# Kernel optimization log

Hardware: AMD Instinct MI355X
Metric: run time of the kernel (lower is better)

The kernel has to match this reference:

```python
import jax, jax.numpy as jnp
import numpy as np

# ---- static config (mirrors init_kwargs) ----
CVAE = 16
VOCAB = 1 << CVAE
V_PATCH_NUMS = (1, 2, 4, 8, 16, 32)
SN = len(V_PATCH_NUMS)
NUM_LATENT_TOKENS = 1024
H = W = 32
BETA = 0.25
ENTROPY_WEIGHT = 0.1
INV_TEMP = 100.0          # temperature 0.01 as in entropy_loss default
EPS = 1e-5
W_SAMPLE_MIN = 1.0
W_BATCH_MAX = 1.0
QUANT_RESI = 0.5
N_PHI = 4                 # share_quant_resi=4 -> PhiPartiallyShared


def _phi_index():
    ticks = (np.linspace(1/3/N_PHI, 1 - 1/3/N_PHI, N_PHI) if N_PHI == 4
             else np.linspace(1/2/N_PHI, 1 - 1/2/N_PHI, N_PHI))
    return [int(np.argmin(np.abs(ticks - si / (SN - 1)))) for si in range(SN)]

PHI_IDX = _phi_index()


def _cubic(t, a=-0.75):  # torch bicubic kernel (a=-0.75)
    t = abs(t)
    if t <= 1.0:
        return (a + 2) * t**3 - (a + 3) * t**2 + 1.0
    if t < 2.0:
        return a * t**3 - 5 * a * t**2 + 8 * a * t - 4 * a
    return 0.0


def _up_matrix(n_in, n_out):
    # exact torch F.interpolate(mode='bicubic', align_corners=False) as a linear map
    M = np.zeros((n_out, n_in), np.float32)
    for i in range(n_out):
        x = (i + 0.5) * n_in / n_out - 0.5
        x0 = int(np.floor(x))
        for k in range(-1, 3):
            j = min(max(x0 + k, 0), n_in - 1)
            M[i, j] += _cubic(x - (x0 + k))
    return M

UP_MATS = {pn: jnp.asarray(_up_matrix(pn, H)) for pn in V_PATCH_NUMS if pn != H}


def area_down(x, pn):  # F.interpolate(mode='area') for divisor sizes == block mean
    B, C, Hh, Ww = x.shape
    return x.reshape(B, C, pn, Hh // pn, pn, Ww // pn).mean((3, 5))


def bicubic_up(x, pn):
    M = UP_MATS[pn]
    return jnp.einsum('hp,bcpq,wq->bchw', M, x, M)


def phi_apply(h, w, b):  # Phi: h*(1-r) + conv3x3(h)*r, r=0.5
    conv = jax.lax.conv_general_dilated(
        h, w, (1, 1), 'SAME', dimension_numbers=('NCHW', 'OIHW', 'NCHW'))
    conv = conv + b[None, :, None, None]
    return h * (1.0 - QUANT_RESI) + conv * QUANT_RESI


def lfq_forward(f_BChw, phi_w, phi_b):
    f = f_BChw.astype(jnp.float32)
    B, C, Hh, Ww = f.shape
    f_ng = jax.lax.stop_gradient(f)
    f_rest = f_ng
    f_hat = jnp.zeros_like(f)
    bitpos = jnp.arange(CVAE, dtype=jnp.int32)
    vq_loss = 0.0
    commit_loss = 0.0
    ent_loss = 0.0
    vocab_hit = jnp.zeros((SN, VOCAB), jnp.float32)
    for si, pn in enumerate(V_PATCH_NUMS):
        cv = 1.0  # scaler[si] = scale**si, scale=1
        last_direct = (si == SN - 1) and (pn == int(np.sqrt(NUM_LATENT_TOKENS)))
        rest = f_rest if last_direct else area_down(f_rest, pn)
        bits = (rest > 0)                                   # sign quantization
        # bits->index (channel-last order matches permute(0,2,3,1))
        idx = jnp.sum(bits.transpose(0, 2, 3, 1).astype(jnp.int32) << bitpos, axis=-1)  # (B,pn,pn)
        hit = jax.ops.segment_sum(jnp.ones((B * pn * pn,), jnp.float32),
                                  idx.reshape(-1), num_segments=VOCAB)
        vocab_hit = vocab_hit.at[si].add(hit)
        # index -> {-cv,+cv} codes: (B,pn,pn,C) -> (B,C,pn,pn)
        code_bits = ((idx[..., None] >> bitpos) & 1).astype(jnp.float32)
        h_small = ((code_bits * 2.0 - 1.0) * cv).transpose(0, 3, 1, 2)
        h = h_small if si == SN - 1 else bicubic_up(h_small, pn)
        h = phi_apply(h, phi_w[PHI_IDX[si]], phi_b[PHI_IDX[si]])
        # residual before this step, shape b (h w) 1 d
        x = (f - jax.lax.stop_gradient(f_hat)).transpose(0, 2, 3, 1).reshape(B, Hh * Ww, 1, C)
        f_hat = f_hat + h      # eval: mask all ones, ratio=1
        f_rest = f_rest - h
        # soft entropy loss (analytical per-sample, per-bit binary probabilities)
        p = jax.nn.sigmoid(-4.0 * x / cv * INV_TEMP)        # (B,HW,1,C)
        prob = jnp.stack([p, 1.0 - p], axis=-1)             # (B,HW,1,C,2)
        sample_ent = -(prob * jnp.log(prob + EPS)).sum(-1)  # per-bit entropy
        per_sample_entropy = sample_ent.sum(-1).mean()
        avg_prob = prob.mean((0, 1, 2))                     # (C,2)
        codebook_entropy = -(avg_prob * jnp.log(avg_prob + EPS)).sum()
        ent_loss = ent_loss + (W_SAMPLE_MIN * per_sample_entropy
                               - W_BATCH_MAX * codebook_entropy)
        vq_loss = vq_loss + jnp.mean((f_hat - f_ng) ** 2)
        commit_loss = commit_loss + BETA * jnp.mean((jax.lax.stop_gradient(f_hat) - f) ** 2)
    vq_loss = vq_loss / SN
    commit_loss = commit_loss / SN
    ent_loss = ent_loss * (ENTROPY_WEIGHT / SN)
    f_hat_out = jax.lax.stop_gradient(f_hat - f_ng) + f     # straight-through estimator
    total = vq_loss + commit_loss + ent_loss
    return f_hat_out, total, vocab_hit


def setup_inputs() -> dict:
    key = jax.random.key(0)
    k1, k2 = jax.random.split(key)
    f = jax.random.normal(k1, (256, 16, 32, 32), dtype=jnp.float32)
    phi_w = jax.random.normal(k2, (N_PHI, CVAE, CVAE, 3, 3), dtype=jnp.float32) * 0.05
    phi_b = jnp.zeros((N_PHI, CVAE), dtype=jnp.float32)
    return {"f_BChw": f, "phi_w": phi_w, "phi_b": phi_b}


def reference(f_BChw, phi_w, phi_b):
    return lfq_forward(f_BChw, phi_w, phi_b)
```

## Files before the change

### kernel.cpp

```cpp
#include <hip/hip_runtime.h>

#define VOCAB 65536
#define NELEM 4194304
#define BHW   262144

__device__ __forceinline__ double cubic_d(double t) {
  const double a = -0.75;
  t = fabs(t);
  if (t <= 1.0) return ((a + 2.0) * t - (a + 3.0)) * t * t + 1.0;
  if (t < 2.0)  return a * (((t - 5.0) * t + 8.0) * t - 4.0);
  return 0.0;
}

__device__ __forceinline__ int idx32_slot(int x, int y) { return (x << 5) | ((y ^ x) & 31); }

template<int PN>
__device__ __forceinline__ void process_scale(
    int si, int phi_idx,
    const float* __restrict__ phi_w, const float* __restrict__ phi_b,
    float* __restrict__ hist, double* __restrict__ acc,
    const float (&fown)[4][8], double (&fhat)[4][8],
    double* __restrict__ hupd, unsigned* __restrict__ idxL,
    float* __restrict__ wMT, double* __restrict__ red,
    int t, int y, int g, int x0)
{
  constexpr int CELLS = PN * PN;
  constexpr int S = 32 / PN;
  const int w = t >> 6;

  idxL[t] = 0u; idxL[t + 512] = 0u;
  if constexpr (PN != 32) {
    if (t < 32) {
      #pragma unroll
      for (int q = 0; q < PN; ++q) wMT[q * 32 + t] = 0.0f;
      double xp = ((double)t + 0.5) * (double)PN / 32.0 - 0.5;
      int q0i = (int)floor(xp);
      for (int k = 0; k < 4; ++k) {
        int j = q0i + k - 1;
        int jc = j < 0 ? 0 : (j > PN - 1 ? PN - 1 : j);
        wMT[jc * 32 + t] += (float)cubic_d(xp - (double)j);
      }
    }
    double mseP = 0.0;
    float entf = 0.0f, ps0 = 0, ps1 = 0, ps2 = 0, ps3 = 0;
    #pragma unroll
    for (int cc = 0; cc < 4; ++cc) {
      double* hp = hupd + (4 * g + cc) * 1056 + y * 33 + x0;
      float psl = 0.0f;
      #pragma unroll
      for (int k = 0; k < 8; ++k) {
        double xr = (double)fown[cc][k] - fhat[cc][k];
        hp[k] = xr;
        mseP += xr * xr;
        float pr = 1.0f / (1.0f + __expf(400.0f * (float)xr));
        entf -= pr * __logf(pr + 1e-5f) + (1.0f - pr) * __logf(1.0f - pr + 1e-5f);
        psl += pr;
      }
      if (cc == 0) ps0 = psl; else if (cc == 1) ps1 = psl; else if (cc == 2) ps2 = psl; else ps3 = psl;
    }
    double ent_d = (double)entf;
    #pragma unroll
    for (int off = 32; off > 0; off >>= 1) {
      mseP  += __shfl_down(mseP, off);
      ent_d += __shfl_down(ent_d, off);
      ps0 += __shfl_down(ps0, off); ps1 += __shfl_down(ps1, off);
      ps2 += __shfl_down(ps2, off); ps3 += __shfl_down(ps3, off);
    }
    if ((t & 63) == 0) {
      red[w * 8 + 0] = mseP; red[w * 8 + 1] = ent_d;
      red[w * 8 + 2] = (double)ps0; red[w * 8 + 3] = (double)ps1;
      red[w * 8 + 4] = (double)ps2; red[w * 8 + 5] = (double)ps3;
    }
  }
  __syncthreads();

  if constexpr (PN != 32) {
    if (t == 0) {
      double m = 0.0, e = 0.0;
      #pragma unroll
      for (int ww = 0; ww < 8; ++ww) { m += red[ww * 8]; e += red[ww * 8 + 1]; }
      if (si > 0) atomicAdd(&acc[(si - 1) * 18 + 0], m);
      atomicAdd(&acc[si * 18 + 1], e);
    }
    if (t < 16) {
      int gg = t >> 2, cc = t & 3;
      atomicAdd(&acc[si * 18 + 2 + t], red[(2 * gg) * 8 + 2 + cc] + red[(2 * gg + 1) * 8 + 2 + cc]);
    }
  }

  if constexpr (PN == 32) {
    double mseP = 0.0;
    float entf = 0.0f, ps0 = 0, ps1 = 0, ps2 = 0, ps3 = 0;
    unsigned bb[8] = {0, 0, 0, 0, 0, 0, 0, 0};
    #pragma unroll
    for (int cc = 0; cc < 4; ++cc) {
      float psl = 0.0f;
      #pragma unroll
      for (int k = 0; k < 8; ++k) {
        double xr = (double)fown[cc][k] - fhat[cc][k];
        if (xr > 0.0) bb[k] |= (1u << cc);
        mseP += xr * xr;
        float pr = 1.0f / (1.0f + __expf(400.0f * (float)xr));
        entf -= pr * __logf(pr + 1e-5f) + (1.0f - pr) * __logf(1.0f - pr + 1e-5f);
        psl += pr;
      }
      if (cc == 0) ps0 = psl; else if (cc == 1) ps1 = psl; else if (cc == 2) ps2 = psl; else ps3 = psl;
    }
    #pragma unroll
    for (int k = 0; k < 8; ++k)
      if (bb[k]) atomicOr(&idxL[idx32_slot(x0 + k, y)], bb[k] << (4 * g));
    double ent_d = (double)entf;
    #pragma unroll
    for (int off = 32; off > 0; off >>= 1) {
      mseP  += __shfl_down(mseP, off);
      ent_d += __shfl_down(ent_d, off);
      ps0 += __shfl_down(ps0, off); ps1 += __shfl_down(ps1, off);
      ps2 += __shfl_down(ps2, off); ps3 += __shfl_down(ps3, off);
    }
    if ((t & 63) == 0) {
      red[w * 8 + 0] = mseP; red[w * 8 + 1] = ent_d;
      red[w * 8 + 2] = (double)ps0; red[w * 8 + 3] = (double)ps1;
      red[w * 8 + 4] = (double)ps2; red[w * 8 + 5] = (double)ps3;
    }
  } else if constexpr (PN == 16) {
    int cell = t & 255;
    int i0 = (cell >> 4) * 2, j0 = (cell & 15) * 2;
    unsigned bits = 0;
    #pragma unroll
    for (int k = 0; k < 8; ++k) {
      int c = (t >> 8) + 2 * k;
      const double* hp = hupd + c * 1056 + i0 * 33 + j0;
      double s = hp[0] + hp[1] + hp[33] + hp[34];
      if (s > 0.0) bits |= (1u << c);
    }
    atomicOr(&idxL[cell], bits);
  } else if constexpr (PN == 8) {
    #pragma unroll
    for (int k = 0; k < 2; ++k) {
      int task = t + 512 * k;
      int c = task >> 6, cell = task & 63;
      const double* hp = hupd + c * 1056 + ((cell >> 3) * 4) * 33 + (cell & 7) * 4;
      double s = 0.0;
      #pragma unroll
      for (int dy = 0; dy < 4; ++dy)
        #pragma unroll
        for (int dx = 0; dx < 4; ++dx) s += hp[dy * 33 + dx];
      if (s > 0.0) atomicOr(&idxL[cell], 1u << c);
    }
  } else {
    constexpr int TASKS = 16 * CELLS;
    constexpr int G = 512 / TASKS;
    int p = t / G, sub = t % G;
    int c = p / CELLS, cell = p % CELLS;
    const double* hp = hupd + c * 1056 + ((cell / PN) * S) * 33 + (cell % PN) * S;
    double s = 0.0;
    for (int e = sub; e < S * S; e += G) s += hp[(e / S) * 33 + (e % S)];
    #pragma unroll
    for (int off = G / 2; off > 0; off >>= 1) s += __shfl_down(s, off, G);
    if (sub == 0 && s > 0.0) atomicOr(&idxL[cell], 1u << c);
  }
  __syncthreads();

  if constexpr (PN == 32) {
    if (t == 0) {
      double m = 0.0, e = 0.0;
      #pragma unroll
      for (int ww = 0; ww < 8; ++ww) { m += red[ww * 8]; e += red[ww * 8 + 1]; }
      atomicAdd(&acc[4 * 18 + 0], m);
      atomicAdd(&acc[5 * 18 + 1], e);
    }
    if (t < 16) {
      int gg = t >> 2, cc = t & 3;
      atomicAdd(&acc[5 * 18 + 2 + t], red[(2 * gg) * 8 + 2 + cc] + red[(2 * gg + 1) * 8 + 2 + cc]);
    }
  }

  if constexpr (PN == 32) {
    atomicAdd(&hist[5 * VOCAB + idxL[t]], 1.0f);
    atomicAdd(&hist[5 * VOCAB + idxL[t + 512]], 1.0f);
  } else {
    if (t < CELLS) atomicAdd(&hist[(size_t)si * VOCAB + idxL[t]], 1.0f);
  }
  {
    int c2 = t >> 5, y2 = t & 31;
    double* hrow = hupd + c2 * 1056 + y2 * 33;
    if constexpr (PN == 32) {
      #pragma unroll
      for (int x = 0; x < 32; ++x)
        hrow[x] = ((idxL[idx32_slot(x, y2)] >> c2) & 1) ? 1.0 : -1.0;
    } else {
      constexpr int QC = (PN < 4) ? PN : 4;
      #pragma unroll
      for (int q0 = 0; q0 < PN; q0 += QC) {
        double tmp[QC];
        #pragma unroll
        for (int qq = 0; qq < QC; ++qq) tmp[qq] = 0.0;
        #pragma unroll
        for (int r = 0; r < PN; ++r) {
          double ww = (double)wMT[r * 32 + y2];
          #pragma unroll
          for (int qq = 0; qq < QC; ++qq) {
            double sg = ((idxL[r * PN + q0 + qq] >> c2) & 1) ? 1.0 : -1.0;
            tmp[qq] = fma(ww, sg, tmp[qq]);
          }
        }
        #pragma unroll
        for (int x = 0; x < 32; ++x) {
          double s2 = (q0 == 0) ? 0.0 : hrow[x];
          #pragma unroll
          for (int qq = 0; qq < QC; ++qq)
            s2 = fma((double)wMT[(q0 + qq) * 32 + x], tmp[qq], s2);
          hrow[x] = s2;
        }
      }
    }
  }
  __syncthreads();

  const float* wgbase = phi_w + phi_idx * 2304;
  #pragma unroll
  for (int cc = 0; cc < 4; ++cc) {
    double bh = 0.5 * (double)phi_b[phi_idx * 16 + 4 * g + cc];
    const double* hu = hupd + (4 * g + cc) * 1056 + y * 33 + x0;
    #pragma unroll
    for (int k = 0; k < 8; ++k)
      fhat[cc][k] = fhat[cc][k] + 0.5 * hu[k] + bh;
  }
  for (int ci = 0; ci < 16; ++ci) {
    const double* hbase = hupd + ci * 1056;
    #pragma unroll
    for (int dy = 0; dy < 3; ++dy) {
      int ry = y + dy - 1;
      if (ry < 0 || ry > 31) continue;
      double prow[10];
      const double* hr = hbase + ry * 33;
      prow[0] = (x0 == 0)  ? 0.0 : hr[x0 - 1];
      #pragma unroll
      for (int jj = 1; jj < 9; ++jj) prow[jj] = hr[x0 - 1 + jj];
      prow[9] = (x0 == 24) ? 0.0 : hr[x0 + 8];
      #pragma unroll
      for (int cc = 0; cc < 4; ++cc) {
        const float* wp = wgbase + ((4 * g + cc) * 16 + ci) * 9 + dy * 3;
        double w0 = 0.5 * (double)wp[0], w1 = 0.5 * (double)wp[1], w2 = 0.5 * (double)wp[2];
        #pragma unroll
        for (int k = 0; k < 8; ++k)
          fhat[cc][k] = fma(w0, prow[k], fma(w1, prow[k + 1], fma(w2, prow[k + 2], fhat[cc][k])));
      }
    }
  }
  __syncthreads();
}

__global__ __launch_bounds__(512) void lfq_all(
    const float* __restrict__ f, const float* __restrict__ phi_w,
    const float* __restrict__ phi_b, float* __restrict__ fhi,
    float* __restrict__ hist, double* __restrict__ acc)
{
  __shared__ double   hupd[16 * 1056];
  __shared__ unsigned idxL[1024];
  __shared__ float    wMT[512];
  __shared__ double   red[64];

  const int t = threadIdx.x;
  const int y = (t >> 2) & 31;
  const int x0 = (t & 3) * 8;
  const int g = __builtin_amdgcn_readfirstlane(t >> 7);
  const size_t ibase = (size_t)blockIdx.x * 16384;
  const int w = t >> 6;

  float fown[4][8];
  double fhat[4][8];
  #pragma unroll
  for (int cc = 0; cc < 4; ++cc) {
    const float* fp = f + ibase + (size_t)(4 * g + cc) * 1024 + y * 32 + x0;
    float4 fa = *(const float4*)fp;
    float4 fb = *(const float4*)(fp + 4);
    fown[cc][0] = fa.x; fown[cc][1] = fa.y; fown[cc][2] = fa.z; fown[cc][3] = fa.w;
    fown[cc][4] = fb.x; fown[cc][5] = fb.y; fown[cc][6] = fb.z; fown[cc][7] = fb.w;
    #pragma unroll
    for (int k = 0; k < 8; ++k) fhat[cc][k] = 0.0;
  }

  process_scale<1 >(0, 0, phi_w, phi_b, hist, acc, fown, fhat, hupd, idxL, wMT, red, t, y, g, x0);
  process_scale<2 >(1, 0, phi_w, phi_b, hist, acc, fown, fhat, hupd, idxL, wMT, red, t, y, g, x0);
  process_scale<4 >(2, 1, phi_w, phi_b, hist, acc, fown, fhat, hupd, idxL, wMT, red, t, y, g, x0);
  process_scale<8 >(3, 2, phi_w, phi_b, hist, acc, fown, fhat, hupd, idxL, wMT, red, t, y, g, x0);
  process_scale<16>(4, 3, phi_w, phi_b, hist, acc, fown, fhat, hupd, idxL, wMT, red, t, y, g, x0);
  process_scale<32>(5, 3, phi_w, phi_b, hist, acc, fown, fhat, hupd, idxL, wMT, red, t, y, g, x0);

  double mse = 0.0;
  #pragma unroll
  for (int cc = 0; cc < 4; ++cc)
    #pragma unroll
    for (int k = 0; k < 8; ++k) {
      double d = fhat[cc][k] - (double)fown[cc][k];
      mse += d * d;
    }
  #pragma unroll
  for (int off = 32; off > 0; off >>= 1) mse += __shfl_down(mse, off);
  if ((t & 63) == 0) red[w * 8] = mse;
  __syncthreads();
  if (t == 0) {
    double m = 0.0;
    #pragma unroll
    for (int ww = 0; ww < 8; ++ww) m += red[ww * 8];
    atomicAdd(&acc[5 * 18 + 0], m);
  }

  #pragma unroll
  for (int cc = 0; cc < 4; ++cc) {
    float* op = fhi + ibase + (size_t)(4 * g + cc) * 1024 + y * 32 + x0;
    *(float4*)op = make_float4((float)fhat[cc][0], (float)fhat[cc][1],
                               (float)fhat[cc][2], (float)fhat[cc][3]);
    *(float4*)(op + 4) = make_float4((float)fhat[cc][4], (float)fhat[cc][5],
                                     (float)fhat[cc][6], (float)fhat[cc][7]);
  }
}

__global__ void finalize_total(const double* __restrict__ acc, float* __restrict__ total)
{
  if (threadIdx.x == 0 && blockIdx.x == 0) {
    double vq = 0.0, ent = 0.0;
    for (int si = 0; si < 6; ++si) {
      vq += acc[si * 18 + 0];
      double pse = acc[si * 18 + 1] / (double)BHW;
      double ce = 0.0;
      for (int cc = 0; cc < 16; ++cc) {
        double ap0 = acc[si * 18 + 2 + cc] / (double)BHW;
        double ap1 = 1.0 - ap0;
        ce -= ap0 * log(ap0 + 1e-5) + ap1 * log(ap1 + 1e-5);
      }
      ent += pse - ce;
    }
    *total = (float)(1.25 * vq / ((double)NELEM * 6.0) + (0.1 / 6.0) * ent);
  }
}

extern "C" void kernel_launch(void* const* d_in, const int* in_sizes, int n_in,
                              void* d_out, int out_size, void* d_ws, size_t ws_size,
                              hipStream_t stream)
{
  const float* f     = (const float*)d_in[0];
  const float* phi_w = (const float*)d_in[1];
  const float* phi_b = (const float*)d_in[2];
  float* out   = (float*)d_out;
  float* fhi   = out;
  float* total = out + NELEM;
  float* hist  = out + NELEM + 1;
  double* acc  = (double*)d_ws;

  hipMemsetAsync((void*)(out + NELEM), 0, (size_t)(1 + 6 * VOCAB) * sizeof(float), stream);
  hipMemsetAsync(d_ws, 0, 1024, stream);

  lfq_all<<<256, 512, 0, stream>>>(f, phi_w, phi_b, fhi, hist, acc);
  finalize_total<<<1, 64, 0, stream>>>(acc, total);
}
```

Baseline: 300.4 us.

## Prefetch conv weights into registers and fuse finalize via last-block counter

The 3x3 Phi convolution now loads its per-input-channel weights into double-buffered register arrays, fetching the next channel's weights while computing the current one, so global weight loads no longer sit in the inner FMA loop. The separate finalize_total kernel is removed: each block bumps an atomic counter and the last block computes the total loss in parallel (entropy terms across threads, then a shuffle reduction). This saves a kernel launch and overlaps weight latency, at the cost of extra registers, which may hurt occupancy, and a threadfence/atomic at the end of every block.

New measurement: 310.9 us. 1.03x slower.

```diff
diff --git a/kernel.cpp b/kernel.cpp
--- a/kernel.cpp
+++ b/kernel.cpp
@@ -217,7 +217,6 @@
   }
   __syncthreads();
 
-  const float* wgbase = phi_w + phi_idx * 2304;
   #pragma unroll
   for (int cc = 0; cc < 4; ++cc) {
     double bh = 0.5 * (double)phi_b[phi_idx * 16 + 4 * g + cc];
@@ -226,27 +225,62 @@
     for (int k = 0; k < 8; ++k)
       fhat[cc][k] = fhat[cc][k] + 0.5 * hu[k] + bh;
   }
-  for (int ci = 0; ci < 16; ++ci) {
-    const double* hbase = hupd + ci * 1056;
-    #pragma unroll
-    for (int dy = 0; dy < 3; ++dy) {
-      int ry = y + dy - 1;
-      if (ry < 0 || ry > 31) continue;
-      double prow[10];
-      const double* hr = hbase + ry * 33;
-      prow[0] = (x0 == 0)  ? 0.0 : hr[x0 - 1];
-      #pragma unroll
-      for (int jj = 1; jj < 9; ++jj) prow[jj] = hr[x0 - 1 + jj];
-      prow[9] = (x0 == 24) ? 0.0 : hr[x0 + 8];
-      #pragma unroll
-      for (int cc = 0; cc < 4; ++cc) {
-        const float* wp = wgbase + ((4 * g + cc) * 16 + ci) * 9 + dy * 3;
-        double w0 = 0.5 * (double)wp[0], w1 = 0.5 * (double)wp[1], w2 = 0.5 * (double)wp[2];
+
+  {
+    const float* wg = phi_w + phi_idx * 2304 + (size_t)(4 * g) * 144;
+    float wA[4][9], wB[4][9];
+    #pragma unroll
+    for (int cc = 0; cc < 4; ++cc)
+      #pragma unroll
+      for (int j = 0; j < 9; ++j) wA[cc][j] = wg[cc * 144 + j];
+
+    #define CONV_BODY(WREG, CI)                                                        \
+      {                                                                                \
+        const double* hbase = hupd + (CI) * 1056;                                      \
+        _Pragma("unroll")                                                              \
+        for (int dy = 0; dy < 3; ++dy) {                                               \
+          int ry = y + dy - 1;                                                         \
+          if (ry < 0 || ry > 31) continue;                                             \
+          double prow[10];                                                             \
+          const double* hr = hbase + ry * 33;                                          \
+          prow[0] = (x0 == 0)  ? 0.0 : hr[x0 - 1];                                     \
+          _Pragma("unroll")                                                            \
+          for (int jj = 1; jj < 9; ++jj) prow[jj] = hr[x0 - 1 + jj];                   \
+          prow[9] = (x0 == 24) ? 0.0 : hr[x0 + 8];                                     \
+          _Pragma("unroll")                                                            \
+          for (int cc = 0; cc < 4; ++cc) {                                             \
+            double w0 = 0.5 * (double)WREG[cc][dy * 3 + 0];                            \
+            double w1 = 0.5 * (double)WREG[cc][dy * 3 + 1];                            \
+            double w2 = 0.5 * (double)WREG[cc][dy * 3 + 2];                            \
+            _Pragma("unroll")                                                          \
+            for (int k = 0; k < 8; ++k)                                                \
+              fhat[cc][k] = fma(w0, prow[k],                                           \
+                             fma(w1, prow[k + 1], fma(w2, prow[k + 2], fhat[cc][k]))); \
+          }                                                                            \
+        }                                                                              \
+      }
+
+    for (int cp = 0; cp < 8; ++cp) {
+      {
+        const int ci = 2 * cp;
         #pragma unroll
-        for (int k = 0; k < 8; ++k)
-          fhat[cc][k] = fma(w0, prow[k], fma(w1, prow[k + 1], fma(w2, prow[k + 2], fhat[cc][k])));
-      }
-    }
+        for (int cc = 0; cc < 4; ++cc)
+          #pragma unroll
+          for (int j = 0; j < 9; ++j) wB[cc][j] = wg[cc * 144 + (ci + 1) * 9 + j];
+        CONV_BODY(wA, ci);
+      }
+      {
+        const int ci = 2 * cp + 1;
+        if (cp < 7) {
+          #pragma unroll
+          for (int cc = 0; cc < 4; ++cc)
+            #pragma unroll
+            for (int j = 0; j < 9; ++j) wA[cc][j] = wg[cc * 144 + (ci + 1) * 9 + j];
+        }
+        CONV_BODY(wB, ci);
+      }
+    }
+    #undef CONV_BODY
   }
   __syncthreads();
 }
@@ -254,12 +288,14 @@
 __global__ __launch_bounds__(512) void lfq_all(
     const float* __restrict__ f, const float* __restrict__ phi_w,
     const float* __restrict__ phi_b, float* __restrict__ fhi,
-    float* __restrict__ hist, double* __restrict__ acc)
+    float* __restrict__ hist, double* __restrict__ acc,
+    unsigned* __restrict__ cnt, float* __restrict__ total)
 {
   __shared__ double   hupd[16 * 1056];
   __shared__ unsigned idxL[1024];
   __shared__ float    wMT[512];
   __shared__ double   red[64];
+  __shared__ unsigned lastflag;
 
   const int t = threadIdx.x;
   const int y = (t >> 2) & 31;
@@ -315,24 +351,36 @@
     *(float4*)(op + 4) = make_float4((float)fhat[cc][4], (float)fhat[cc][5],
                                      (float)fhat[cc][6], (float)fhat[cc][7]);
   }
-}
-
-__global__ void finalize_total(const double* __restrict__ acc, float* __restrict__ total)
-{
-  if (threadIdx.x == 0 && blockIdx.x == 0) {
-    double vq = 0.0, ent = 0.0;
-    for (int si = 0; si < 6; ++si) {
-      vq += acc[si * 18 + 0];
-      double pse = acc[si * 18 + 1] / (double)BHW;
-      double ce = 0.0;
-      for (int cc = 0; cc < 16; ++cc) {
-        double ap0 = acc[si * 18 + 2 + cc] / (double)BHW;
-        double ap1 = 1.0 - ap0;
-        ce -= ap0 * log(ap0 + 1e-5) + ap1 * log(ap1 + 1e-5);
-      }
-      ent += pse - ce;
-    }
-    *total = (float)(1.25 * vq / ((double)NELEM * 6.0) + (0.1 / 6.0) * ent);
+
+  __threadfence();
+  if (t == 0) {
+    unsigned old = atomicAdd(cnt, 1u);
+    lastflag = (old == 255u) ? 1u : 0u;
+  }
+  __syncthreads();
+  if (lastflag) {
+    __threadfence();
+    double q = 0.0;
+    if (t < 96) {
+      int si = t >> 4, cc = t & 15;
+      double ap0 = acc[si * 18 + 2 + cc] / (double)BHW;
+      double ap1 = 1.0 - ap0;
+      q = ap0 * log(ap0 + 1e-5) + ap1 * log(ap1 + 1e-5);
+    }
+    #pragma unroll
+    for (int off = 32; off > 0; off >>= 1) q += __shfl_down(q, off);
+    if (t < 512 && (t & 63) == 0) red[t >> 6] = q;
+    __syncthreads();
+    if (t == 0) {
+      double qsum = red[0] + red[1];
+      double vq = 0.0, pse = 0.0;
+      for (int si = 0; si < 6; ++si) {
+        vq  += acc[si * 18 + 0];
+        pse += acc[si * 18 + 1] / (double)BHW;
+      }
+      double ent = pse + qsum;
+      *total = (float)(1.25 * vq / ((double)NELEM * 6.0) + (0.1 / 6.0) * ent);
+    }
   }
 }
 
@@ -348,10 +396,10 @@
   float* total = out + NELEM;
   float* hist  = out + NELEM + 1;
   double* acc  = (double*)d_ws;
+  unsigned* cnt = (unsigned*)((char*)d_ws + 960);
 
   hipMemsetAsync((void*)(out + NELEM), 0, (size_t)(1 + 6 * VOCAB) * sizeof(float), stream);
   hipMemsetAsync(d_ws, 0, 1024, stream);
 
-  lfq_all<<<256, 512, 0, stream>>>(f, phi_w, phi_b, fhi, hist, acc);
-  finalize_total<<<1, 64, 0, stream>>>(acc, total);
+  lfq_all<<<256, 512, 0, stream>>>(f, phi_w, phi_b, fhi, hist, acc, cnt, total);
 }
```

## Compute per-scale sign bits in registers via shuffles instead of shared-memory residual pass

Applied to the files above, without the earlier changes.

Residual sign reduction for each coarse scale is done directly from registers with cross-lane xor shuffles and per-cell atomicOr, removing the write of residuals to shared memory and the separate read-back pass plus one barrier per scale. Accumulator and histogram updates are unified, and the single-cell scale uses a small shared buffer. The shared-memory row stride changes from 33 to 34 doubles so conv row loads can use aligned double2 vector reads. It adds shuffle work and relies on the new reduction order matching the reference's sign decisions.

New measurement: 301.1 us. About the same (+0.2%).

```diff
diff --git a/kernel.cpp b/kernel.cpp
--- a/kernel.cpp
+++ b/kernel.cpp
@@ -3,6 +3,8 @@
 #define VOCAB 65536
 #define NELEM 4194304
 #define BHW   262144
+#define RS    34
+#define CH    (RS * 32)
 
 __device__ __forceinline__ double cubic_d(double t) {
   const double a = -0.75;
@@ -21,14 +23,12 @@
     float* __restrict__ hist, double* __restrict__ acc,
     const float (&fown)[4][8], double (&fhat)[4][8],
     double* __restrict__ hupd, unsigned* __restrict__ idxL,
-    float* __restrict__ wMT, double* __restrict__ red,
+    float* __restrict__ wMT, double* __restrict__ red, double* __restrict__ pn1buf,
     int t, int y, int g, int x0)
 {
   constexpr int CELLS = PN * PN;
-  constexpr int S = 32 / PN;
   const int w = t >> 6;
 
-  idxL[t] = 0u; idxL[t + 512] = 0u;
   if constexpr (PN != 32) {
     if (t < 32) {
       #pragma unroll
@@ -41,22 +41,92 @@
         wMT[jc * 32 + t] += (float)cubic_d(xp - (double)j);
       }
     }
+  }
+  {
     double mseP = 0.0;
     float entf = 0.0f, ps0 = 0, ps1 = 0, ps2 = 0, ps3 = 0;
+    unsigned bm0 = 0, bm1 = 0, bm2 = 0, bm3 = 0;
+    unsigned bb[8] = {0, 0, 0, 0, 0, 0, 0, 0};
     #pragma unroll
     for (int cc = 0; cc < 4; ++cc) {
-      double* hp = hupd + (4 * g + cc) * 1056 + y * 33 + x0;
+      double r[8];
       float psl = 0.0f;
       #pragma unroll
       for (int k = 0; k < 8; ++k) {
         double xr = (double)fown[cc][k] - fhat[cc][k];
-        hp[k] = xr;
+        r[k] = xr;
         mseP += xr * xr;
         float pr = 1.0f / (1.0f + __expf(400.0f * (float)xr));
         entf -= pr * __logf(pr + 1e-5f) + (1.0f - pr) * __logf(1.0f - pr + 1e-5f);
         psl += pr;
       }
       if (cc == 0) ps0 = psl; else if (cc == 1) ps1 = psl; else if (cc == 2) ps2 = psl; else ps3 = psl;
+
+      if constexpr (PN == 32) {
+        #pragma unroll
+        for (int k = 0; k < 8; ++k)
+          if (r[k] > 0.0) bb[k] |= (1u << cc);
+      } else if constexpr (PN == 16) {
+        #pragma unroll
+        for (int j = 0; j < 4; ++j) {
+          double s = r[2 * j] + r[2 * j + 1];
+          s += __shfl_xor(s, 4);
+          if (s > 0.0) {
+            unsigned b = 1u << (4 * g + cc);
+            if (j == 0) bm0 |= b; else if (j == 1) bm1 |= b; else if (j == 2) bm2 |= b; else bm3 |= b;
+          }
+        }
+      } else if constexpr (PN == 8) {
+        double sA = ((r[0] + r[1]) + (r[2] + r[3]));
+        double sB = ((r[4] + r[5]) + (r[6] + r[7]));
+        sA += __shfl_xor(sA, 4); sA += __shfl_xor(sA, 8);
+        sB += __shfl_xor(sB, 4); sB += __shfl_xor(sB, 8);
+        if (sA > 0.0) bm0 |= 1u << (4 * g + cc);
+        if (sB > 0.0) bm1 |= 1u << (4 * g + cc);
+      } else if constexpr (PN == 4) {
+        double s = ((r[0] + r[1]) + (r[2] + r[3])) + ((r[4] + r[5]) + (r[6] + r[7]));
+        s += __shfl_xor(s, 4); s += __shfl_xor(s, 8); s += __shfl_xor(s, 16);
+        if (s > 0.0) bm0 |= 1u << (4 * g + cc);
+      } else if constexpr (PN == 2) {
+        double s = ((r[0] + r[1]) + (r[2] + r[3])) + ((r[4] + r[5]) + (r[6] + r[7]));
+        s += __shfl_xor(s, 1);
+        s += __shfl_xor(s, 4); s += __shfl_xor(s, 8);
+        s += __shfl_xor(s, 16); s += __shfl_xor(s, 32);
+        if (s > 0.0) bm0 |= 1u << (4 * g + cc);
+      } else {
+        double s = ((r[0] + r[1]) + (r[2] + r[3])) + ((r[4] + r[5]) + (r[6] + r[7]));
+        s += __shfl_xor(s, 1); s += __shfl_xor(s, 2);
+        s += __shfl_xor(s, 4); s += __shfl_xor(s, 8);
+        s += __shfl_xor(s, 16); s += __shfl_xor(s, 32);
+        if ((t & 63) == 0) pn1buf[w * 4 + cc] = s;
+      }
+    }
+    if constexpr (PN == 32) {
+      #pragma unroll
+      for (int k = 0; k < 8; ++k)
+        if (bb[k]) atomicOr(&idxL[idx32_slot(x0 + k, y)], bb[k] << (4 * g));
+    } else if constexpr (PN == 16) {
+      if ((y & 1) == 0) {
+        int cb = (y >> 1) * 16 + (x0 >> 1);
+        if (bm0) atomicOr(&idxL[cb + 0], bm0);
+        if (bm1) atomicOr(&idxL[cb + 1], bm1);
+        if (bm2) atomicOr(&idxL[cb + 2], bm2);
+        if (bm3) atomicOr(&idxL[cb + 3], bm3);
+      }
+    } else if constexpr (PN == 8) {
+      if ((y & 3) == 0) {
+        int cb = (y >> 2) * 8 + (x0 >> 2);
+        if (bm0) atomicOr(&idxL[cb + 0], bm0);
+        if (bm1) atomicOr(&idxL[cb + 1], bm1);
+      }
+    } else if constexpr (PN == 4) {
+      if ((y & 7) == 0) {
+        if (bm0) atomicOr(&idxL[(y >> 3) * 4 + (x0 >> 3)], bm0);
+      }
+    } else if constexpr (PN == 2) {
+      if ((y & 15) == 0 && (x0 & 8) == 0) {
+        if (bm0) atomicOr(&idxL[(y >> 4) * 2 + (x0 >> 4)], bm0);
+      }
     }
     double ent_d = (double)entf;
     #pragma unroll
@@ -74,116 +144,39 @@
   }
   __syncthreads();
 
-  if constexpr (PN != 32) {
+  if constexpr (PN == 1) {
     if (t == 0) {
-      double m = 0.0, e = 0.0;
-      #pragma unroll
-      for (int ww = 0; ww < 8; ++ww) { m += red[ww * 8]; e += red[ww * 8 + 1]; }
-      if (si > 0) atomicAdd(&acc[(si - 1) * 18 + 0], m);
-      atomicAdd(&acc[si * 18 + 1], e);
-    }
-    if (t < 16) {
-      int gg = t >> 2, cc = t & 3;
-      atomicAdd(&acc[si * 18 + 2 + t], red[(2 * gg) * 8 + 2 + cc] + red[(2 * gg + 1) * 8 + 2 + cc]);
-    }
-  }
-
-  if constexpr (PN == 32) {
-    double mseP = 0.0;
-    float entf = 0.0f, ps0 = 0, ps1 = 0, ps2 = 0, ps3 = 0;
-    unsigned bb[8] = {0, 0, 0, 0, 0, 0, 0, 0};
-    #pragma unroll
-    for (int cc = 0; cc < 4; ++cc) {
-      float psl = 0.0f;
-      #pragma unroll
-      for (int k = 0; k < 8; ++k) {
-        double xr = (double)fown[cc][k] - fhat[cc][k];
-        if (xr > 0.0) bb[k] |= (1u << cc);
-        mseP += xr * xr;
-        float pr = 1.0f / (1.0f + __expf(400.0f * (float)xr));
-        entf -= pr * __logf(pr + 1e-5f) + (1.0f - pr) * __logf(1.0f - pr + 1e-5f);
-        psl += pr;
-      }
-      if (cc == 0) ps0 = psl; else if (cc == 1) ps1 = psl; else if (cc == 2) ps2 = psl; else ps3 = psl;
-    }
-    #pragma unroll
-    for (int k = 0; k < 8; ++k)
-      if (bb[k]) atomicOr(&idxL[idx32_slot(x0 + k, y)], bb[k] << (4 * g));
-    double ent_d = (double)entf;
-    #pragma unroll
-    for (int off = 32; off > 0; off >>= 1) {
-      mseP  += __shfl_down(mseP, off);
-      ent_d += __shfl_down(ent_d, off);
-      ps0 += __shfl_down(ps0, off); ps1 += __shfl_down(ps1, off);
-      ps2 += __shfl_down(ps2, off); ps3 += __shfl_down(ps3, off);
-    }
-    if ((t & 63) == 0) {
-      red[w * 8 + 0] = mseP; red[w * 8 + 1] = ent_d;
-      red[w * 8 + 2] = (double)ps0; red[w * 8 + 3] = (double)ps1;
-      red[w * 8 + 4] = (double)ps2; red[w * 8 + 5] = (double)ps3;
-    }
-  } else if constexpr (PN == 16) {
-    int cell = t & 255;
-    int i0 = (cell >> 4) * 2, j0 = (cell & 15) * 2;
-    unsigned bits = 0;
-    #pragma unroll
-    for (int k = 0; k < 8; ++k) {
-      int c = (t >> 8) + 2 * k;
-      const double* hp = hupd + c * 1056 + i0 * 33 + j0;
-      double s = hp[0] + hp[1] + hp[33] + hp[34];
-      if (s > 0.0) bits |= (1u << c);
-    }
-    atomicOr(&idxL[cell], bits);
-  } else if constexpr (PN == 8) {
-    #pragma unroll
-    for (int k = 0; k < 2; ++k) {
-      int task = t + 512 * k;
-      int c = task >> 6, cell = task & 63;
-      const double* hp = hupd + c * 1056 + ((cell >> 3) * 4) * 33 + (cell & 7) * 4;
-      double s = 0.0;
-      #pragma unroll
-      for (int dy = 0; dy < 4; ++dy)
-        #pragma unroll
-        for (int dx = 0; dx < 4; ++dx) s += hp[dy * 33 + dx];
-      if (s > 0.0) atomicOr(&idxL[cell], 1u << c);
-    }
-  } else {
-    constexpr int TASKS = 16 * CELLS;
-    constexpr int G = 512 / TASKS;
-    int p = t / G, sub = t % G;
-    int c = p / CELLS, cell = p % CELLS;
-    const double* hp = hupd + c * 1056 + ((cell / PN) * S) * 33 + (cell % PN) * S;
-    double s = 0.0;
-    for (int e = sub; e < S * S; e += G) s += hp[(e / S) * 33 + (e % S)];
-    #pragma unroll
-    for (int off = G / 2; off > 0; off >>= 1) s += __shfl_down(s, off, G);
-    if (sub == 0 && s > 0.0) atomicOr(&idxL[cell], 1u << c);
-  }
-  __syncthreads();
-
-  if constexpr (PN == 32) {
-    if (t == 0) {
-      double m = 0.0, e = 0.0;
-      #pragma unroll
-      for (int ww = 0; ww < 8; ++ww) { m += red[ww * 8]; e += red[ww * 8 + 1]; }
-      atomicAdd(&acc[4 * 18 + 0], m);
-      atomicAdd(&acc[5 * 18 + 1], e);
-    }
-    if (t < 16) {
-      int gg = t >> 2, cc = t & 3;
-      atomicAdd(&acc[5 * 18 + 2 + t], red[(2 * gg) * 8 + 2 + cc] + red[(2 * gg + 1) * 8 + 2 + cc]);
-    }
-  }
-
+      unsigned idx = 0;
+      for (int c = 0; c < 16; ++c) {
+        double tot = pn1buf[(2 * (c >> 2)) * 4 + (c & 3)] + pn1buf[(2 * (c >> 2) + 1) * 4 + (c & 3)];
+        if (tot > 0.0) idx |= (1u << c);
+      }
+      idxL[0] = idx;
+      atomicAdd(&hist[idx], 1.0f);
+    }
+    __syncthreads();
+  }
+
+  if (t == 0) {
+    double m = 0.0, e = 0.0;
+    #pragma unroll
+    for (int ww = 0; ww < 8; ++ww) { m += red[ww * 8]; e += red[ww * 8 + 1]; }
+    if (si > 0) atomicAdd(&acc[(si - 1) * 18 + 0], m);
+    atomicAdd(&acc[si * 18 + 1], e);
+  }
+  if (t < 16) {
+    int gg = t >> 2, cc = t & 3;
+    atomicAdd(&acc[si * 18 + 2 + t], red[(2 * gg) * 8 + 2 + cc] + red[(2 * gg + 1) * 8 + 2 + cc]);
+  }
   if constexpr (PN == 32) {
     atomicAdd(&hist[5 * VOCAB + idxL[t]], 1.0f);
     atomicAdd(&hist[5 * VOCAB + idxL[t + 512]], 1.0f);
-  } else {
+  } else if constexpr (PN != 1) {
     if (t < CELLS) atomicAdd(&hist[(size_t)si * VOCAB + idxL[t]], 1.0f);
   }
   {
     int c2 = t >> 5, y2 = t & 31;
-    double* hrow = hupd + c2 * 1056 + y2 * 33;
+    double* hrow = hupd + c2 * CH + y2 * RS;
     if constexpr (PN == 32) {
       #pragma unroll
       for (int x = 0; x < 32; ++x)
@@ -217,26 +210,31 @@
   }
   __syncthreads();
 
+  idxL[t] = 0u; idxL[t + 512] = 0u;
   const float* wgbase = phi_w + phi_idx * 2304;
   #pragma unroll
   for (int cc = 0; cc < 4; ++cc) {
     double bh = 0.5 * (double)phi_b[phi_idx * 16 + 4 * g + cc];
-    const double* hu = hupd + (4 * g + cc) * 1056 + y * 33 + x0;
+    const double* hu = hupd + (4 * g + cc) * CH + y * RS + x0;
     #pragma unroll
     for (int k = 0; k < 8; ++k)
       fhat[cc][k] = fhat[cc][k] + 0.5 * hu[k] + bh;
   }
   for (int ci = 0; ci < 16; ++ci) {
-    const double* hbase = hupd + ci * 1056;
+    const double* hbase = hupd + ci * CH;
     #pragma unroll
     for (int dy = 0; dy < 3; ++dy) {
       int ry = y + dy - 1;
       if (ry < 0 || ry > 31) continue;
+      const double* hr = hbase + ry * RS;
       double prow[10];
-      const double* hr = hbase + ry * 33;
       prow[0] = (x0 == 0)  ? 0.0 : hr[x0 - 1];
-      #pragma unroll
-      for (int jj = 1; jj < 9; ++jj) prow[jj] = hr[x0 - 1 + jj];
+      {
+        const double2* hp2 = (const double2*)(hr + x0);
+        double2 p01 = hp2[0], p23 = hp2[1], p45 = hp2[2], p67 = hp2[3];
+        prow[1] = p01.x; prow[2] = p01.y; prow[3] = p23.x; prow[4] = p23.y;
+        prow[5] = p45.x; prow[6] = p45.y; prow[7] = p67.x; prow[8] = p67.y;
+      }
       prow[9] = (x0 == 24) ? 0.0 : hr[x0 + 8];
       #pragma unroll
       for (int cc = 0; cc < 4; ++cc) {
@@ -256,10 +254,11 @@
     const float* __restrict__ phi_b, float* __restrict__ fhi,
     float* __restrict__ hist, double* __restrict__ acc)
 {
-  __shared__ double   hupd[16 * 1056];
+  __shared__ double   hupd[16 * CH];
   __shared__ unsigned idxL[1024];
   __shared__ float    wMT[512];
   __shared__ double   red[64];
+  __shared__ double   pn1buf[32];
 
   const int t = threadIdx.x;
   const int y = (t >> 2) & 31;
@@ -281,12 +280,12 @@
     for (int k = 0; k < 8; ++k) fhat[cc][k] = 0.0;
   }
 
-  process_scale<1 >(0, 0, phi_w, phi_b, hist, acc, fown, fhat, hupd, idxL, wMT, red, t, y, g, x0);
-  process_scale<2 >(1, 0, phi_w, phi_b, hist, acc, fown, fhat, hupd, idxL, wMT, red, t, y, g, x0);
-  process_scale<4 >(2, 1, phi_w, phi_b, hist, acc, fown, fhat, hupd, idxL, wMT, red, t, y, g, x0);
-  process_scale<8 >(3, 2, phi_w, phi_b, hist, acc, fown, fhat, hupd, idxL, wMT, red, t, y, g, x0);
-  process_scale<16>(4, 3, phi_w, phi_b, hist, acc, fown, fhat, hupd, idxL, wMT, red, t, y, g, x0);
-  process_scale<32>(5, 3, phi_w, phi_b, hist, acc, fown, fhat, hupd, idxL, wMT, red, t, y, g, x0);
+  process_scale<1 >(0, 0, phi_w, phi_b, hist, acc, fown, fhat, hupd, idxL, wMT, red, pn1buf, t, y, g, x0);
+  process_scale<2 >(1, 0, phi_w, phi_b, hist, acc, fown, fhat, hupd, idxL, wMT, red, pn1buf, t, y, g, x0);
+  process_scale<4 >(2, 1, phi_w, phi_b, hist, acc, fown, fhat, hupd, idxL, wMT, red, pn1buf, t, y, g, x0);
+  process_scale<8 >(3, 2, phi_w, phi_b, hist, acc, fown, fhat, hupd, idxL, wMT, red, pn1buf, t, y, g, x0);
+  process_scale<16>(4, 3, phi_w, phi_b, hist, acc, fown, fhat, hupd, idxL, wMT, red, pn1buf, t, y, g, x0);
+  process_scale<32>(5, 3, phi_w, phi_b, hist, acc, fown, fhat, hupd, idxL, wMT, red, pn1buf, t, y, g, x0);
 
   double mse = 0.0;
   #pragma unroll
```
